# Kernel optimization log

Measured on AMD Instinct MI355X. Metric: run time of the kernel, lower is better.

## Reference

```python
import jax, jax.numpy as jnp
import numpy as np

DIM = 1024
HEADS = 16
HEAD_DIM = DIM // HEADS
HIDDEN = DIM * 4
EPS = 1e-6


def _layernorm(x, g, b):
    mu = jnp.mean(x, axis=-1, keepdims=True)
    var = jnp.mean(jnp.square(x - mu), axis=-1, keepdims=True)
    return (x - mu) * jax.lax.rsqrt(var + EPS) * g + b


def setup_inputs() -> dict:
    key = jax.random.key(0)
    ks = jax.random.split(key, 12)
    s = 0.02
    return {
        "x": jax.random.normal(ks[0], (16, 1024, DIM), dtype=jnp.float32),
        "ln1_g": jnp.ones((DIM,), jnp.float32),
        "ln1_b": jnp.zeros((DIM,), jnp.float32),
        "qkv_w": jax.random.normal(ks[1], (DIM, 3 * DIM), jnp.float32) * s,
        "qkv_b": jnp.zeros((3 * DIM,), jnp.float32),
        "proj_w": jax.random.normal(ks[2], (DIM, DIM), jnp.float32) * s,
        "proj_b": jnp.zeros((DIM,), jnp.float32),
        "ls1_g": jnp.ones((DIM,), jnp.float32),
        "ln2_g": jnp.ones((DIM,), jnp.float32),
        "ln2_b": jnp.zeros((DIM,), jnp.float32),
        "fc1_w": jax.random.normal(ks[3], (DIM, HIDDEN), jnp.float32) * s,
        "fc1_b": jnp.zeros((HIDDEN,), jnp.float32),
        "fc2_w": jax.random.normal(ks[4], (HIDDEN, DIM), jnp.float32) * s,
        "fc2_b": jnp.zeros((DIM,), jnp.float32),
        "ls2_g": jnp.ones((DIM,), jnp.float32),
    }


def reference(x, ln1_g, ln1_b, qkv_w, qkv_b, proj_w, proj_b, ls1_g,
              ln2_g, ln2_b, fc1_w, fc1_b, fc2_w, fc2_b, ls2_g):
    B, N, C = x.shape
    # --- attention branch (NOTE: original code omits 1/sqrt(d) scaling) ---
    h = _layernorm(x, ln1_g, ln1_b)
    qkv = (h @ qkv_w + qkv_b).reshape(B, N, 3, HEADS, HEAD_DIM)
    q, k, v = jnp.moveaxis(qkv, 2, 0)          # each [B, N, H, D]
    attn = jnp.einsum("bqhd,bkhd->bhqk", q, k)  # no scale, faithful to source
    attn = jax.nn.softmax(attn, axis=-1)
    out = jnp.einsum("bhqk,bkhd->bqhd", attn, v).reshape(B, N, C)
    x = x + (out @ proj_w + proj_b) * ls1_g
    # --- MLP branch ---
    h = _layernorm(x, ln2_g, ln2_b)
    h = jax.nn.gelu(h @ fc1_w + fc1_b, approximate=False)
    x = x + (h @ fc2_w + fc2_b) * ls2_g
    return x
```

## Files before the change

### kernel.cpp

```cpp
#include <hip/hip_runtime.h>
#include <hip/hip_bf16.h>
#include <math.h>

typedef __attribute__((ext_vector_type(8))) short short8;
typedef __attribute__((ext_vector_type(4))) float f32x4;

#define MFMA16(a,b,c) __builtin_amdgcn_mfma_f32_16x16x32_bf16((a),(b),(c),0,0,0)

__device__ __forceinline__ unsigned short f2bf(float f){
  unsigned int u = __builtin_bit_cast(unsigned int, f);
  u += 0x7fffu + ((u >> 16) & 1u);
  return (unsigned short)(u >> 16);
}

__device__ __forceinline__ void gload16(const void* g, void* lds){
  __builtin_amdgcn_global_load_lds(
      (const __attribute__((address_space(1))) unsigned int*)g,
      (__attribute__((address_space(3))) unsigned int*)lds, 16, 0, 0);
}

__global__ __launch_bounds__(256) void k_transpose_cast(const float* __restrict__ in,
    unsigned short* __restrict__ out, int K, int N)
{
  __shared__ unsigned short tile[32][33];
  const int tx = threadIdx.x, ty = threadIdx.y;
  const int n0 = blockIdx.x * 32, k0 = blockIdx.y * 32;
  #pragma unroll
  for (int i = 0; i < 4; i++) {
    int k = k0 + ty + i*8;
    tile[ty + i*8][tx] = f2bf(in[(size_t)k * N + n0 + tx]);
  }
  __syncthreads();
  #pragma unroll
  for (int i = 0; i < 4; i++) {
    int n = n0 + ty + i*8;
    out[(size_t)n * K + k0 + tx] = tile[tx][ty + i*8];
  }
}

__global__ __launch_bounds__(256) void k_layernorm(const float* __restrict__ x,
    const float* __restrict__ g, const float* __restrict__ b,
    unsigned short* __restrict__ out)
{
  const int row = blockIdx.x;
  const int t = threadIdx.x;
  const float4 v = ((const float4*)(x + (size_t)row * 1024))[t];
  float s  = v.x + v.y + v.z + v.w;
  float s2 = v.x*v.x + v.y*v.y + v.z*v.z + v.w*v.w;
  #pragma unroll
  for (int m = 1; m < 64; m <<= 1) {
    s  += __shfl_xor(s,  m);
    s2 += __shfl_xor(s2, m);
  }
  __shared__ float red[2][4];
  const int wid = t >> 6, lane = t & 63;
  if (lane == 0) { red[0][wid] = s; red[1][wid] = s2; }
  __syncthreads();
  s  = red[0][0] + red[0][1] + red[0][2] + red[0][3];
  s2 = red[1][0] + red[1][1] + red[1][2] + red[1][3];
  const float mu = s * (1.0f / 1024.0f);
  const float var = s2 * (1.0f / 1024.0f) - mu * mu;
  const float rstd = rsqrtf(var + 1e-6f);
  const float4 gv = ((const float4*)g)[t];
  const float4 bv = ((const float4*)b)[t];
  ushort4 o;
  o.x = f2bf((v.x - mu) * rstd * gv.x + bv.x);
  o.y = f2bf((v.y - mu) * rstd * gv.y + bv.y);
  o.z = f2bf((v.z - mu) * rstd * gv.z + bv.z);
  o.w = f2bf((v.w - mu) * rstd * gv.w + bv.w);
  ((ushort4*)(out + (size_t)row * 1024))[t] = o;
}

template<int EPI>
__global__ __launch_bounds__(512, 2) void k_gemm256(
    const unsigned short* __restrict__ A,
    const unsigned short* __restrict__ Bt,
    const float* __restrict__ bias,
    const float* __restrict__ resid,
    const float* __restrict__ lsg,
    void* __restrict__ outp,
    unsigned short* __restrict__ vtp,
    int M, int N, int K, int nbn)
{
  __shared__ __align__(16) char smem[131072];

  const int bid = blockIdx.x;
  const int mrows = (gridDim.x >> 3) / nbn;
  const int xcd = bid & 7, l = bid >> 3;
  const int bm = xcd * mrows + (l % mrows);
  const int bn = l / mrows;

  const int t = threadIdx.x, lane = t & 63;
  const int wid = t >> 6, wm = wid >> 2, wn = wid & 3;
  const int fr = lane & 15, fg = lane >> 4;

  const int rowL = t >> 3;
  const int cs8 = ((t & 7) ^ (rowL & 7)) * 8;
  const size_t aBase = ((size_t)bm * 256 + rowL) * K + cs8;
  const size_t bBase = ((size_t)bn * 256 + rowL) * K + cs8;

#define STG_A(rowb, bb, X) gload16(A  + aBase + (size_t)(rowb)*K + (size_t)(X)*64, \
                                   smem + (bb)*32768 + (rowb)*128 + t*16)
#define STG_B(rowb, bb, X) gload16(Bt + bBase + (size_t)(rowb)*K + (size_t)(X)*64, \
                                   smem + 65536 + (bb)*32768 + (rowb)*128 + t*16)
#define STG_A4(bb, X) { STG_A(0,bb,X); STG_A(64,bb,X); STG_A(128,bb,X); STG_A(192,bb,X); }
#define STG_B4(bb, X) { STG_B(0,bb,X); STG_B(64,bb,X); STG_B(128,bb,X); STG_B(192,bb,X); }

#define RD_AF(mh, bb) \
  _Pragma("unroll") \
  for (int m_ = 0; m_ < 4; m_++) { \
    const int row_ = wm*128 + (mh)*64 + m_*16 + fr; \
    const unsigned short* p_ = (const unsigned short*)smem + (bb)*16384 + row_*64; \
    af[m_*2+0] = *(const short8*)&p_[((fg)   ^ (row_&7))*8]; \
    af[m_*2+1] = *(const short8*)&p_[((4+fg) ^ (row_&7))*8]; \
  }

#define RD_BF(bb) \
  _Pragma("unroll") \
  for (int n_ = 0; n_ < 4; n_++) { \
    const int row_ = wn*64 + n_*16 + fr; \
    const unsigned short* p_ = (const unsigned short*)(smem + 65536) + (bb)*16384 + row_*64; \
    bfv[n_*2+0] = *(const short8*)&p_[((fg)   ^ (row_&7))*8]; \
    bfv[n_*2+1] = *(const short8*)&p_[((4+fg) ^ (row_&7))*8]; \
  }

#define MMAH(mh) \
  __builtin_amdgcn_s_setprio(1); \
  _Pragma("unroll") \
  for (int kk_ = 0; kk_ < 2; kk_++) \
    _Pragma("unroll") \
    for (int m_ = 0; m_ < 4; m_++) \
      _Pragma("unroll") \
      for (int n_ = 0; n_ < 4; n_++) \
        acc[(mh)*4+m_][n_] = MFMA16(af[m_*2+kk_], bfv[n_*2+kk_], acc[(mh)*4+m_][n_]); \
  __builtin_amdgcn_s_setprio(0);

#define BAR asm volatile("s_barrier" ::: "memory")

  f32x4 acc[8][4] = {};
  short8 af[8], bfv[8];
  const int NT = K >> 6;

  STG_A4(0, 0);
  STG_B4(0, 0);
  STG_A4(1, 1);

  for (int j = 0; j < (NT >> 1); ++j) {
    const int T = 2 * j;
    const bool more  = (T + 2 < NT);
    const bool more3 = (T + 3 < NT);
    STG_B4(1, T + 1);
    asm volatile("s_waitcnt vmcnt(8)" ::: "memory");
    BAR;
    RD_AF(0, 0); RD_BF(0);
    MMAH(0);
    BAR;
    RD_AF(1, 0);
    if (more) STG_A4(0, T + 2);
    BAR;
    MMAH(1);
    BAR;
    if (more) {
      STG_B4(0, T + 2);
      asm volatile("s_waitcnt vmcnt(8)" ::: "memory");
    } else {
      asm volatile("s_waitcnt vmcnt(0)" ::: "memory");
    }
    BAR;
    RD_AF(0, 1); RD_BF(1);
    MMAH(0);
    BAR;
    RD_AF(1, 1);
    if (more3) STG_A4(1, T + 3);
    BAR;
    MMAH(1);
    BAR;
  }

  const int row0 = bm * 256 + wm * 128 + fg * 4;
  const int col0 = bn * 256 + wn * 64 + fr;
  #pragma unroll
  for (int n = 0; n < 4; n++) {
    const int col = col0 + n * 16;
    const float bcol = bias[col];
    float lscale = 0.f;
    if (EPI == 2) lscale = lsg[col];
    #pragma unroll
    for (int m = 0; m < 8; m++) {
      #pragma unroll
      for (int r = 0; r < 4; r++) {
        const int row = row0 + m * 16 + r;
        float v = acc[m][n][r] + bcol;
        if (EPI == 0) {
          if (bn < 8) {
            ((unsigned short*)outp)[(size_t)row * 2048 + col] = f2bf(v);
          } else {
            const int d = col - 2048, hh = d >> 6, dd = d & 63;
            const int bb = row >> 10, nn = row & 1023;
            vtp[(((size_t)bb * 16 + hh) * 64 + dd) * 1024 + nn] = f2bf(v);
          }
        } else if (EPI == 1) {
          const float u = v * (0.7978845608f + 0.0356774081f * v * v);
          v = v * __builtin_amdgcn_rcpf(1.0f + __expf(-2.0f * u));
          ((unsigned short*)outp)[(size_t)row * N + col] = f2bf(v);
        } else {
          ((float*)outp)[(size_t)row * N + col] =
              resid[(size_t)row * N + col] + v * lscale;
        }
      }
    }
  }
#undef STG_A
#undef STG_B
#undef STG_A4
#undef STG_B4
#undef RD_AF
#undef RD_BF
#undef MMAH
#undef BAR
}

__global__ __launch_bounds__(512) void k_attn(const unsigned short* __restrict__ qk,
                                              const unsigned short* __restrict__ vT,
                                              unsigned short* __restrict__ out)
{
  const int qt = blockIdx.x;
  const int bh = blockIdx.y;
  const int b = bh >> 4, h = bh & 15;
  const int t = threadIdx.x, lane = t & 63, wid = t >> 6;
  const int fr = lane & 15, fg = lane >> 4;
  const int q0 = qt * 256 + wid * 32;

  __shared__ __align__(16) unsigned short Ksm[64 * 64];
  __shared__ __align__(16) unsigned short Vsm[64 * 64];
  __shared__ __align__(16) unsigned short plds[8][32][72];

  const size_t qbase = (size_t)b * 1024 * 2048 + (size_t)h * 64;
  const size_t kbase = qbase + 1024;
  const size_t vbase = (size_t)bh * 64 * 1024;

  short8 qf[2][2];
  #pragma unroll
  for (int m = 0; m < 2; m++)
    #pragma unroll
    for (int kh = 0; kh < 2; kh++)
      qf[m][kh] = *(const short8*)(qk + qbase + (size_t)(q0 + m*16 + fr) * 2048
                                   + kh*32 + fg*8);

  f32x4 oacc[2][4] = {};
  float mrow[2][4], lrow[2][4];
  #pragma unroll
  for (int m = 0; m < 2; m++)
    #pragma unroll
    for (int r = 0; r < 4; r++) { mrow[m][r] = -1e30f; lrow[m][r] = 0.f; }

  const int srow = t >> 3, sc = t & 7;
  const int scs = sc ^ (srow & 7);

  for (int kv0 = 0; kv0 < 1024; kv0 += 64) {
    __syncthreads();
    gload16(qk + kbase + (size_t)(kv0 + srow) * 2048 + scs*8, (char*)Ksm + t*16);
    gload16(vT + vbase + (size_t)srow * 1024 + kv0 + scs*8,   (char*)Vsm + t*16);
    __syncthreads();

    f32x4 sacc[2][4] = {};
    #pragma unroll
    for (int n = 0; n < 4; n++) {
      #pragma unroll
      for (int kh = 0; kh < 2; kh++) {
        const int krow = n*16 + fr;
        short8 kf = *(const short8*)&Ksm[krow*64 + (((kh*4 + fg) ^ (krow & 7)) * 8)];
        sacc[0][n] = MFMA16(qf[0][kh], kf, sacc[0][n]);
        sacc[1][n] = MFMA16(qf[1][kh], kf, sacc[1][n]);
      }
    }

    #pragma unroll
    for (int m = 0; m < 2; m++) {
      float pm[4];
      #pragma unroll
      for (int r = 0; r < 4; r++)
        pm[r] = fmaxf(fmaxf(sacc[m][0][r], sacc[m][1][r]),
                      fmaxf(sacc[m][2][r], sacc[m][3][r]));
      #pragma unroll
      for (int msk = 1; msk < 16; msk <<= 1)
        #pragma unroll
        for (int r = 0; r < 4; r++) pm[r] = fmaxf(pm[r], __shfl_xor(pm[r], msk));
      float corr[4];
      #pragma unroll
      for (int r = 0; r < 4; r++) {
        float mn = fmaxf(mrow[m][r], pm[r]);
        corr[r] = __expf(mrow[m][r] - mn);
        mrow[m][r] = mn;
      }
      float psum[4] = {0.f, 0.f, 0.f, 0.f};
      #pragma unroll
      for (int n = 0; n < 4; n++)
        #pragma unroll
        for (int r = 0; r < 4; r++) {
          float p = __expf(sacc[m][n][r] - mrow[m][r]);
          sacc[m][n][r] = p;
          psum[r] += p;
        }
      #pragma unroll
      for (int msk = 1; msk < 16; msk <<= 1)
        #pragma unroll
        for (int r = 0; r < 4; r++) psum[r] += __shfl_xor(psum[r], msk);
      #pragma unroll
      for (int r = 0; r < 4; r++) lrow[m][r] = lrow[m][r] * corr[r] + psum[r];
      #pragma unroll
      for (int d16 = 0; d16 < 4; d16++)
        #pragma unroll
        for (int r = 0; r < 4; r++) oacc[m][d16][r] *= corr[r];
      #pragma unroll
      for (int n = 0; n < 4; n++)
        #pragma unroll
        for (int r = 0; r < 4; r++)
          plds[wid][m*16 + fg*4 + r][n*16 + fr] = f2bf(sacc[m][n][r]);
    }

    short8 pf[2][2];
    #pragma unroll
    for (int m = 0; m < 2; m++)
      #pragma unroll
      for (int kh = 0; kh < 2; kh++)
        pf[m][kh] = *(const short8*)&plds[wid][m*16 + fr][kh*32 + fg*8];

    #pragma unroll
    for (int d16 = 0; d16 < 4; d16++) {
      #pragma unroll
      for (int kh = 0; kh < 2; kh++) {
        const int vrow = d16*16 + fr;
        short8 vf = *(const short8*)&Vsm[vrow*64 + (((kh*4 + fg) ^ (vrow & 7)) * 8)];
        oacc[0][d16] = MFMA16(pf[0][kh], vf, oacc[0][d16]);
        oacc[1][d16] = MFMA16(pf[1][kh], vf, oacc[1][d16]);
      }
    }
  }

  #pragma unroll
  for (int m = 0; m < 2; m++) {
    float inv[4];
    #pragma unroll
    for (int r = 0; r < 4; r++) inv[r] = 1.0f / lrow[m][r];
    #pragma unroll
    for (int d16 = 0; d16 < 4; d16++) {
      #pragma unroll
      for (int r = 0; r < 4; r++) {
        const int qrow = q0 + m*16 + fg*4 + r;
        const int col = h*64 + d16*16 + fr;
        out[(size_t)(b * 1024 + qrow) * 1024 + col] = f2bf(oacc[m][d16][r] * inv[r]);
      }
    }
  }
}

extern "C" void kernel_launch(void* const* d_in, const int* in_sizes, int n_in,
                              void* d_out, int out_size, void* d_ws, size_t ws_size,
                              hipStream_t stream) {
  const float* x      = (const float*)d_in[0];
  const float* ln1_g  = (const float*)d_in[1];
  const float* ln1_b  = (const float*)d_in[2];
  const float* qkv_w  = (const float*)d_in[3];
  const float* qkv_b  = (const float*)d_in[4];
  const float* proj_w = (const float*)d_in[5];
  const float* proj_b = (const float*)d_in[6];
  const float* ls1_g  = (const float*)d_in[7];
  const float* ln2_g  = (const float*)d_in[8];
  const float* ln2_b  = (const float*)d_in[9];
  const float* fc1_w  = (const float*)d_in[10];
  const float* fc1_b  = (const float*)d_in[11];
  const float* fc2_w  = (const float*)d_in[12];
  const float* fc2_b  = (const float*)d_in[13];
  const float* ls2_g  = (const float*)d_in[14];

  char* w = (char*)d_ws;
  unsigned short* wqkvT  = (unsigned short*)(w + 0);
  unsigned short* wprojT = (unsigned short*)(w + 6291456);
  unsigned short* wfc1T  = (unsigned short*)(w + 8388608);
  unsigned short* wfc2T  = (unsigned short*)(w + 16777216);
  float*          x1     = (float*)(w + 25165824);
  unsigned short* h1     = (unsigned short*)(w + 92274688);
  unsigned short* qkbuf  = (unsigned short*)(w + 125829120);
  unsigned short* vtbuf  = (unsigned short*)(w + 192937984);
  unsigned short* attno  = (unsigned short*)(w + 226492416);
  unsigned short* h3     = (unsigned short*)(w + 125829120);

  dim3 tb32(32, 8);
  k_transpose_cast<<<dim3(3072/32, 1024/32), tb32, 0, stream>>>(qkv_w,  wqkvT, 1024, 3072);
  k_transpose_cast<<<dim3(1024/32, 1024/32), tb32, 0, stream>>>(proj_w, wprojT, 1024, 1024);
  k_transpose_cast<<<dim3(4096/32, 1024/32), tb32, 0, stream>>>(fc1_w,  wfc1T, 1024, 4096);
  k_transpose_cast<<<dim3(1024/32, 4096/32), tb32, 0, stream>>>(fc2_w,  wfc2T, 4096, 1024);

  k_layernorm<<<16384, 256, 0, stream>>>(x, ln1_g, ln1_b, h1);
  k_gemm256<0><<<64*12, 512, 0, stream>>>(h1, wqkvT, qkv_b, nullptr, nullptr,
                                          qkbuf, vtbuf, 16384, 3072, 1024, 12);
  k_attn<<<dim3(4, 256), 512, 0, stream>>>(qkbuf, vtbuf, attno);
  k_gemm256<2><<<64*4, 512, 0, stream>>>(attno, wprojT, proj_b, x, ls1_g,
                                         x1, nullptr, 16384, 1024, 1024, 4);
  k_layernorm<<<16384, 256, 0, stream>>>(x1, ln2_g, ln2_b, h1);
  k_gemm256<1><<<64*16, 512, 0, stream>>>(h1, wfc1T, fc1_b, nullptr, nullptr,
                                          h3, nullptr, 16384, 4096, 1024, 16);
  k_gemm256<2><<<64*4, 512, 0, stream>>>(h3, wfc2T, fc2_b, x1, ls2_g,
                                         (float*)d_out, nullptr, 16384, 1024, 4096, 4);
}
```

Measured before the change: 834.0 us.

## Restructure GEMM main loop into 8-phase quadrant schedule with half-tile LDS staging

Reorganizes the 256x256 bf16 GEMM main loop so each 64-deep K tile is computed as four quadrant MFMA phases (m-half x n-half), with the global-to-LDS loads split into 128-row halves and interleaved between phases. The LDS layout changes so each wave's A and B halves occupy contiguous 16KB regions, and the B fragments are double-buffered in registers (bf0/bf1). Barrier-plus-lgkmcnt-plus-sched_barrier sync points are used to overlap loads with MFMA more finely. It adds more barriers per iteration and more complex vmcnt bookkeeping, which risks extra synchronization overhead or ordering hazards.

```diff
diff --git a/kernel.cpp b/kernel.cpp
--- a/kernel.cpp
+++ b/kernel.cpp
@@ -94,87 +94,98 @@
   const int wid = t >> 6, wm = wid >> 2, wn = wid & 3;
   const int fr = lane & 15, fg = lane >> 4;
 
-  const int rowL = t >> 3;
-  const int cs8 = ((t & 7) ^ (rowL & 7)) * 8;
-  const size_t aBase = ((size_t)bm * 256 + rowL) * K + cs8;
-  const size_t bBase = ((size_t)bn * 256 + rowL) * K + cs8;
-
-#define STG_A(rowb, bb, X) gload16(A  + aBase + (size_t)(rowb)*K + (size_t)(X)*64, \
-                                   smem + (bb)*32768 + (rowb)*128 + t*16)
-#define STG_B(rowb, bb, X) gload16(Bt + bBase + (size_t)(rowb)*K + (size_t)(X)*64, \
-                                   smem + 65536 + (bb)*32768 + (rowb)*128 + t*16)
-#define STG_A4(bb, X) { STG_A(0,bb,X); STG_A(64,bb,X); STG_A(128,bb,X); STG_A(192,bb,X); }
-#define STG_B4(bb, X) { STG_B(0,bb,X); STG_B(64,bb,X); STG_B(128,bb,X); STG_B(192,bb,X); }
-
-#define RD_AF(mh, bb) \
+  const int hr0 = t >> 3;
+  const int cs0 = ((t & 7) ^ (hr0 & 7)) * 8;
+  const int hr1 = (512 + t) >> 3;
+  const int cs1 = (((512 + t) & 7) ^ (hr1 & 7)) * 8;
+  const size_t aR0 = ((size_t)bm * 256 + hr0) * K + cs0;
+  const size_t aR1 = ((size_t)bm * 256 + hr1) * K + cs1;
+  const size_t bR0 = ((size_t)bn * 256 + hr0) * K + cs0;
+  const size_t bR1 = ((size_t)bn * 256 + hr1) * K + cs1;
+
+#define STG_A(h, bb, X) { \
+  gload16(A + aR0 + (size_t)(h)*128*K + (size_t)(X)*64, smem + ((bb)*2+(h))*16384 + t*16); \
+  gload16(A + aR1 + (size_t)(h)*128*K + (size_t)(X)*64, smem + ((bb)*2+(h))*16384 + 8192 + t*16); }
+#define STG_B(h, bb, X) { \
+  gload16(Bt + bR0 + (size_t)(h)*128*K + (size_t)(X)*64, smem + 65536 + ((bb)*2+(h))*16384 + t*16); \
+  gload16(Bt + bR1 + (size_t)(h)*128*K + (size_t)(X)*64, smem + 65536 + ((bb)*2+(h))*16384 + 8192 + t*16); }
+
+#define RD_AF(mhq, bb) \
   _Pragma("unroll") \
   for (int m_ = 0; m_ < 4; m_++) { \
-    const int row_ = wm*128 + (mh)*64 + m_*16 + fr; \
-    const unsigned short* p_ = (const unsigned short*)smem + (bb)*16384 + row_*64; \
-    af[m_*2+0] = *(const short8*)&p_[((fg)   ^ (row_&7))*8]; \
-    af[m_*2+1] = *(const short8*)&p_[((4+fg) ^ (row_&7))*8]; \
-  }
-
-#define RD_BF(bb) \
+    const int rr_ = (mhq)*64 + m_*16 + fr; \
+    const char* p_ = smem + ((bb)*2 + wm)*16384 + rr_*128; \
+    af[m_*2+0] = *(const short8*)(p_ + ((fg ^ (fr&7))*16)); \
+    af[m_*2+1] = *(const short8*)(p_ + (((4+fg) ^ (fr&7))*16)); \
+  }
+#define RD_BF(nhq, bb, dst) \
   _Pragma("unroll") \
-  for (int n_ = 0; n_ < 4; n_++) { \
-    const int row_ = wn*64 + n_*16 + fr; \
-    const unsigned short* p_ = (const unsigned short*)(smem + 65536) + (bb)*16384 + row_*64; \
-    bfv[n_*2+0] = *(const short8*)&p_[((fg)   ^ (row_&7))*8]; \
-    bfv[n_*2+1] = *(const short8*)&p_[((4+fg) ^ (row_&7))*8]; \
-  }
-
-#define MMAH(mh) \
+  for (int n_ = 0; n_ < 2; n_++) { \
+    const int rr_ = (wn&1)*64 + (nhq)*32 + n_*16 + fr; \
+    const char* p_ = smem + 65536 + ((bb)*2 + (wn>>1))*16384 + rr_*128; \
+    dst[n_*2+0] = *(const short8*)(p_ + ((fg ^ (fr&7))*16)); \
+    dst[n_*2+1] = *(const short8*)(p_ + (((4+fg) ^ (fr&7))*16)); \
+  }
+
+#define MMAQ(mhq, nhq, B_) \
   __builtin_amdgcn_s_setprio(1); \
   _Pragma("unroll") \
   for (int kk_ = 0; kk_ < 2; kk_++) \
     _Pragma("unroll") \
     for (int m_ = 0; m_ < 4; m_++) \
       _Pragma("unroll") \
-      for (int n_ = 0; n_ < 4; n_++) \
-        acc[(mh)*4+m_][n_] = MFMA16(af[m_*2+kk_], bfv[n_*2+kk_], acc[(mh)*4+m_][n_]); \
+      for (int n_ = 0; n_ < 2; n_++) \
+        acc[(mhq)*4+m_][(nhq)*2+n_] = \
+            MFMA16(af[m_*2+kk_], B_[n_*2+kk_], acc[(mhq)*4+m_][(nhq)*2+n_]); \
   __builtin_amdgcn_s_setprio(0);
 
-#define BAR asm volatile("s_barrier" ::: "memory")
+#define PH_SYNC \
+  __builtin_amdgcn_s_barrier(); \
+  asm volatile("s_waitcnt lgkmcnt(0)" ::: "memory"); \
+  __builtin_amdgcn_sched_barrier(0);
+#define PH_END __builtin_amdgcn_s_barrier();
 
   f32x4 acc[8][4] = {};
-  short8 af[8], bfv[8];
+  short8 af[8], bf0[4], bf1[4];
   const int NT = K >> 6;
 
-  STG_A4(0, 0);
-  STG_B4(0, 0);
-  STG_A4(1, 1);
+  STG_B(0, 0, 0); STG_B(1, 0, 0); STG_A(0, 0, 0); STG_A(1, 0, 0);
+  STG_B(0, 1, 1); STG_B(1, 1, 1); STG_A(0, 1, 1);
+  asm volatile("s_waitcnt vmcnt(6)" ::: "memory");
+  __builtin_amdgcn_s_barrier();
 
   for (int j = 0; j < (NT >> 1); ++j) {
     const int T = 2 * j;
-    const bool more  = (T + 2 < NT);
-    const bool more3 = (T + 3 < NT);
-    STG_B4(1, T + 1);
-    asm volatile("s_waitcnt vmcnt(8)" ::: "memory");
-    BAR;
-    RD_AF(0, 0); RD_BF(0);
-    MMAH(0);
-    BAR;
+    const bool more = (T + 2 < NT);
+    RD_AF(0, 0); RD_BF(0, 0, bf0);
+    STG_A(1, 1, T + 1);
+    PH_SYNC; MMAQ(0, 0, bf0); PH_END;
+    RD_BF(1, 0, bf1);
+    PH_SYNC; MMAQ(0, 1, bf1); PH_END;
     RD_AF(1, 0);
-    if (more) STG_A4(0, T + 2);
-    BAR;
-    MMAH(1);
-    BAR;
+    if (more) STG_B(0, 0, T + 2);
+    PH_SYNC; MMAQ(1, 0, bf0); PH_END;
     if (more) {
-      STG_B4(0, T + 2);
-      asm volatile("s_waitcnt vmcnt(8)" ::: "memory");
+      STG_B(1, 0, T + 2);
+      asm volatile("s_waitcnt vmcnt(4)" ::: "memory");
     } else {
       asm volatile("s_waitcnt vmcnt(0)" ::: "memory");
     }
-    BAR;
-    RD_AF(0, 1); RD_BF(1);
-    MMAH(0);
-    BAR;
+    PH_SYNC; MMAQ(1, 1, bf1); PH_END;
+    RD_AF(0, 1); RD_BF(0, 1, bf0);
+    if (more) STG_A(0, 0, T + 2);
+    PH_SYNC; MMAQ(0, 0, bf0); PH_END;
+    RD_BF(1, 1, bf1);
+    if (more) STG_A(1, 0, T + 2);
+    PH_SYNC; MMAQ(0, 1, bf1); PH_END;
     RD_AF(1, 1);
-    if (more3) STG_A4(1, T + 3);
-    BAR;
-    MMAH(1);
-    BAR;
+    if (more) STG_B(0, 1, T + 3);
+    PH_SYNC; MMAQ(1, 0, bf0); PH_END;
+    if (more) {
+      STG_B(1, 1, T + 3); STG_A(0, 1, T + 3);
+      asm volatile("s_waitcnt vmcnt(6)" ::: "memory");
+    }
+    PH_SYNC; MMAQ(1, 1, bf1); PH_END;
   }
 
   const int row0 = bm * 256 + wm * 128 + fg * 4;
@@ -212,12 +223,11 @@
   }
 #undef STG_A
 #undef STG_B
-#undef STG_A4
-#undef STG_B4
 #undef RD_AF
 #undef RD_BF
-#undef MMAH
-#undef BAR
+#undef MMAQ
+#undef PH_SYNC
+#undef PH_END
 }
 
 __global__ __launch_bounds__(512) void k_attn(const unsigned short* __restrict__ qk,
```

Measured after the change: 838.8 us. Within noise of the previous version (+0.6%).
